# Kernel optimization log

Measured on AMD Instinct MI355X. Metric: run time of the kernel, lower is better.

## Reference

```python
import jax, jax.numpy as jnp
import numpy as np

N, E = 50000, 800000
IN_DIM = 128
OUT_DIM = 128
H = 8
D = OUT_DIM // H  # head_dim = 16
LN_EPS = 1e-5


def setup_inputs() -> dict:
    key = jax.random.key(0)
    ks = jax.random.split(key, 16)
    s_in = 1.0 / np.sqrt(IN_DIM)
    s_out = 1.0 / np.sqrt(OUT_DIM)
    return {
        "x": jax.random.normal(ks[0], (N, IN_DIM), dtype=jnp.float32),
        "edge_index": jax.random.randint(ks[1], (2, E), 0, N, dtype=jnp.int32),
        "edge_attr": jax.random.uniform(ks[2], (E,), dtype=jnp.float32),
        # per-head TransformerConv params, stacked over heads (heads=1 per conv)
        "Wq": jax.random.normal(ks[3], (H, IN_DIM, D), dtype=jnp.float32) * s_in,
        "bq": jnp.zeros((H, D), dtype=jnp.float32),
        "Wk": jax.random.normal(ks[4], (H, IN_DIM, D), dtype=jnp.float32) * s_in,
        "bk": jnp.zeros((H, D), dtype=jnp.float32),
        "Wv": jax.random.normal(ks[5], (H, IN_DIM, D), dtype=jnp.float32) * s_in,
        "bv": jnp.zeros((H, D), dtype=jnp.float32),
        "We": jax.random.normal(ks[6], (H, D), dtype=jnp.float32),  # lin_edge (edge_dim=1, no bias)
        "Wskip": jax.random.normal(ks[7], (H, IN_DIM, D), dtype=jnp.float32) * s_in,
        "bskip": jnp.zeros((H, D), dtype=jnp.float32),
        "Wo": jax.random.normal(ks[8], (OUT_DIM, OUT_DIM), dtype=jnp.float32) * s_out,
        "bo": jnp.zeros((OUT_DIM,), dtype=jnp.float32),
        "gamma": jnp.ones((OUT_DIM,), dtype=jnp.float32),
        "beta": jnp.zeros((OUT_DIM,), dtype=jnp.float32),
    }


def reference(x, edge_index, edge_attr, Wq, bq, Wk, bk, Wv, bv, We, Wskip, bskip, Wo, bo, gamma, beta):
    n = x.shape[0]
    h, _, d = Wq.shape
    src, dst = edge_index[0], edge_index[1]
    # node-level projections for all heads at once: [N, H, D]
    q = jnp.einsum('ni,hid->nhd', x, Wq) + bq
    k = jnp.einsum('ni,hid->nhd', x, Wk) + bk
    v = jnp.einsum('ni,hid->nhd', x, Wv) + bv
    # edge embedding: lin_edge on scalar edge_attr -> [E, H, D]
    e = edge_attr[:, None, None] * We[None, :, :]
    # attention logits per edge/head: q_dst . (k_src + e) / sqrt(d)
    ke = k[src] + e
    alpha = jnp.einsum('ehd,ehd->eh', q[dst], ke) / jnp.sqrt(jnp.asarray(d, x.dtype))
    # segment softmax over destination nodes
    m = jax.ops.segment_max(alpha, dst, num_segments=n)  # [N, H]
    m = jnp.where(jnp.isfinite(m), m, 0.0)
    ex = jnp.exp(alpha - m[dst])
    denom = jax.ops.segment_sum(ex, dst, num_segments=n)
    w = ex / jnp.maximum(denom[dst], 1e-16)  # [E, H]
    # weighted aggregation of (v_src + e)
    agg = jax.ops.segment_sum(w[:, :, None] * (v[src] + e), dst, num_segments=n)  # [N, H, D]
    # root/skip connection inside each TransformerConv
    skip = jnp.einsum('ni,hid->nhd', x, Wskip) + bskip
    heads_cat = (agg + skip).reshape(n, h * d)  # concat over heads -> [N, OUT_DIM]
    out = heads_cat @ Wo + bo
    out = out + x  # residual (in_dim == out_dim)
    mu = out.mean(-1, keepdims=True)
    var = out.var(-1, keepdims=True)
    out = (out - mu) * jax.lax.rsqrt(var + LN_EPS) * gamma + beta
    return out
```

## Files before the change

kernel.cpp:

```cpp
#include <hip/hip_runtime.h>
#include <hip/hip_bf16.h>
#include <stdint.h>
#include <math.h>

#define IN_DIM 128
#define H_HEADS 8
#define HD 16

typedef __attribute__((ext_vector_type(8))) short bf16x8;
typedef __attribute__((ext_vector_type(4))) float f32x4;

__device__ __forceinline__ unsigned short f2bf(float f) {
    __hip_bfloat16 h = __float2bfloat16(f);
    return reinterpret_cast<unsigned short&>(h);
}
__device__ __forceinline__ float bf2f(unsigned short h) {
    return __uint_as_float(((unsigned int)h) << 16);
}

__device__ __forceinline__ void split_f8(const float4 f0, const float4 f1,
                                         bf16x8& h8, bf16x8& l8) {
    float ff[8] = {f0.x, f0.y, f0.z, f0.w, f1.x, f1.y, f1.z, f1.w};
    union { bf16x8 v; unsigned short u[8]; } H, L;
#pragma unroll
    for (int j = 0; j < 8; ++j) {
        H.u[j] = f2bf(ff[j]);
        L.u[j] = f2bf(ff[j] - bf2f(H.u[j]));
    }
    h8 = H.v; l8 = L.v;
}

__device__ __forceinline__ void stage_B(const unsigned short* __restrict__ src,
                                        unsigned short* __restrict__ lds, int t)
{
#pragma unroll
    for (int j = 0; j < 8; ++j) {
        int idx16 = t + j * 256;
        int c = idx16 >> 4, kcol = idx16 & 15;
        uint4 v = *reinterpret_cast<const uint4*>(src + (size_t)c * 128 + kcol * 8);
        *reinterpret_cast<uint4*>(lds + c * 128 + ((kcol ^ (c & 15)) * 8)) = v;
    }
}
__device__ __forceinline__ bf16x8 read_B(const unsigned short* __restrict__ lds,
                                         int c, int kcol)
{
    return *reinterpret_cast<const bf16x8*>(lds + c * 128 + ((kcol ^ (c & 15)) * 8));
}

__global__ __launch_bounds__(256)
void prep_count_kernel(const float* __restrict__ Wq, const float* __restrict__ Wk,
                       const float* __restrict__ Wv, const float* __restrict__ Wsk,
                       const float* __restrict__ Wo,
                       const float* __restrict__ bq, const float* __restrict__ bk,
                       const float* __restrict__ bv, const float* __restrict__ bsk,
                       unsigned short* __restrict__ WtH, unsigned short* __restrict__ WtL,
                       float* __restrict__ bias_cat,
                       const int* __restrict__ ei, int* __restrict__ deg, int E)
{
    const int b = blockIdx.x;
    const int t = threadIdx.x;
    if (b >= 5) {
        int e = (b - 5) * 256 + t;
        if (e < E) atomicAdd(&deg[ei[E + e]], 1);
        return;
    }
    const int p = b;
    const float* src = (p == 0) ? Wq : (p == 1) ? Wk : (p == 2) ? Wv : (p == 3) ? Wsk : Wo;
    unsigned short* dh = WtH + (size_t)p * 16384;
    unsigned short* dl = WtL + (size_t)p * 16384;
#pragma unroll
    for (int j = 0; j < 64; ++j) {
        int o = t + j * 256;
        int c = o >> 7, k = o & 127;
        float v;
        if (p < 4) {
            int h = c >> 4, d = c & 15;
            v = src[(size_t)h * 2048 + (size_t)k * 16 + d];
        } else {
            v = src[(size_t)k * 128 + c];
        }
        unsigned short hi = f2bf(v);
        unsigned short lo = f2bf(v - bf2f(hi));
        dh[o] = hi; dl[o] = lo;
    }
    if (p < 4 && t < 128) {
        const float* bb = (p == 0) ? bq : (p == 1) ? bk : (p == 2) ? bv : bsk;
        bias_cat[p * 128 + t] = bb[t];
    }
}

__global__ __launch_bounds__(256)
void gemm_proj_kernel(const float* __restrict__ A,
                      const unsigned short* __restrict__ WtH_base,
                      const unsigned short* __restrict__ WtL_base,
                      const float* __restrict__ bias_cat,
                      float* __restrict__ qout, float* __restrict__ skipout,
                      unsigned short* __restrict__ kvout, int N)
{
    __shared__ unsigned short Bs[16384];
    const int t = threadIdx.x;
    const int lane = t & 63;
    const int w = t >> 6;
    const int lr = lane & 15;
    const int lk = lane >> 4;
    const int p = blockIdx.y;
    const int brow0 = blockIdx.x * 64 + w * 16;
    const int arow = min(brow0 + lr, N - 1);
    const float* ap = A + (size_t)arow * 128;

    bf16x8 ah[4], al[4];
#pragma unroll
    for (int ks = 0; ks < 4; ++ks) {
        float4 f0 = *reinterpret_cast<const float4*>(ap + ks * 32 + lk * 8);
        float4 f1 = *reinterpret_cast<const float4*>(ap + ks * 32 + lk * 8 + 4);
        split_f8(f0, f1, ah[ks], al[ks]);
    }

    f32x4 acc[8];
#pragma unroll
    for (int ni = 0; ni < 8; ++ni) acc[ni] = (f32x4){0.f, 0.f, 0.f, 0.f};

    stage_B(WtH_base + (size_t)p * 16384, Bs, t);
    __syncthreads();
#pragma unroll
    for (int ks = 0; ks < 4; ++ks)
#pragma unroll
        for (int ni = 0; ni < 8; ++ni) {
            bf16x8 bh = read_B(Bs, ni * 16 + lr, ks * 4 + lk);
            acc[ni] = __builtin_amdgcn_mfma_f32_16x16x32_bf16(ah[ks], bh, acc[ni], 0, 0, 0);
            acc[ni] = __builtin_amdgcn_mfma_f32_16x16x32_bf16(al[ks], bh, acc[ni], 0, 0, 0);
        }
    __syncthreads();
    stage_B(WtL_base + (size_t)p * 16384, Bs, t);
    __syncthreads();
#pragma unroll
    for (int ks = 0; ks < 4; ++ks)
#pragma unroll
        for (int ni = 0; ni < 8; ++ni) {
            bf16x8 bl = read_B(Bs, ni * 16 + lr, ks * 4 + lk);
            acc[ni] = __builtin_amdgcn_mfma_f32_16x16x32_bf16(ah[ks], bl, acc[ni], 0, 0, 0);
        }

    const float* bias = bias_cat + p * 128;
    if (p == 0 || p == 3) {
        float* outp = (p == 0) ? qout : skipout;
#pragma unroll
        for (int ni = 0; ni < 8; ++ni) {
            int col = ni * 16 + lr;
            float bc = bias[col];
#pragma unroll
            for (int r = 0; r < 4; ++r) {
                int gr = brow0 + lk * 4 + r;
                if (gr < N) outp[(size_t)gr * 128 + col] = acc[ni][r] + bc;
            }
        }
    } else {
        unsigned int* kvu = (unsigned int*)kvout;
        const int slot = (p == 1) ? 0 : 1;
#pragma unroll
        for (int ni = 0; ni < 8; ++ni) {
            int col = ni * 16 + lr;
            float bc = bias[col];
#pragma unroll
            for (int r = 0; r < 4; ++r) {
                unsigned int s = f2bf(acc[ni][r] + bc);
                unsigned int o = __shfl_xor((int)s, 1);
                int gr = brow0 + lk * 4 + r;
                if (((lr & 1) == 0) && gr < N)
                    kvu[(size_t)gr * 128 + 2 * (col >> 1) + slot] = s | (o << 16);
            }
        }
    }
}

__global__ __launch_bounds__(256)
void gemm_out_ln_kernel(const float* __restrict__ A,
                        const unsigned short* __restrict__ BtH_t,
                        const unsigned short* __restrict__ BtL_t,
                        const float* __restrict__ bo,
                        const float* __restrict__ res,
                        const float* __restrict__ gamma,
                        const float* __restrict__ beta,
                        float* __restrict__ out, int N)
{
    __shared__ unsigned short Bs[16384];
    __shared__ float lnS[2][32], lnSq[2][32];
    const int t = threadIdx.x;
    const int lane = t & 63;
    const int w = t >> 6;
    const int lr = lane & 15;
    const int lk = lane >> 4;
    const int ch = w & 1;
    const int rg = w >> 1;
    const int brow0 = blockIdx.x * 32 + rg * 16;
    const int arow = min(brow0 + lr, N - 1);
    const float* ap = A + (size_t)arow * 128;

    bf16x8 ah[4], al[4];
#pragma unroll
    for (int ks = 0; ks < 4; ++ks) {
        float4 f0 = *reinterpret_cast<const float4*>(ap + ks * 32 + lk * 8);
        float4 f1 = *reinterpret_cast<const float4*>(ap + ks * 32 + lk * 8 + 4);
        split_f8(f0, f1, ah[ks], al[ks]);
    }

    f32x4 acc[4];
#pragma unroll
    for (int ni = 0; ni < 4; ++ni) acc[ni] = (f32x4){0.f, 0.f, 0.f, 0.f};

    stage_B(BtH_t, Bs, t);
    __syncthreads();
#pragma unroll
    for (int ks = 0; ks < 4; ++ks)
#pragma unroll
        for (int ni = 0; ni < 4; ++ni) {
            bf16x8 bh = read_B(Bs, ch * 64 + ni * 16 + lr, ks * 4 + lk);
            acc[ni] = __builtin_amdgcn_mfma_f32_16x16x32_bf16(ah[ks], bh, acc[ni], 0, 0, 0);
            acc[ni] = __builtin_amdgcn_mfma_f32_16x16x32_bf16(al[ks], bh, acc[ni], 0, 0, 0);
        }
    __syncthreads();
    stage_B(BtL_t, Bs, t);
    __syncthreads();
#pragma unroll
    for (int ks = 0; ks < 4; ++ks)
#pragma unroll
        for (int ni = 0; ni < 4; ++ni) {
            bf16x8 bl = read_B(Bs, ch * 64 + ni * 16 + lr, ks * 4 + lk);
            acc[ni] = __builtin_amdgcn_mfma_f32_16x16x32_bf16(ah[ks], bl, acc[ni], 0, 0, 0);
        }

#pragma unroll
    for (int ni = 0; ni < 4; ++ni) {
        int col = ch * 64 + ni * 16 + lr;
        float bc = bo[col];
#pragma unroll
        for (int r = 0; r < 4; ++r) {
            int gr = brow0 + lk * 4 + r;
            float rv = (gr < N) ? res[(size_t)gr * 128 + col] : 0.f;
            acc[ni][r] += bc + rv;
        }
    }
    float ps[4], pq[4];
#pragma unroll
    for (int r = 0; r < 4; ++r) {
        float s = 0.f, sq = 0.f;
#pragma unroll
        for (int ni = 0; ni < 4; ++ni) { float v = acc[ni][r]; s += v; sq += v * v; }
#pragma unroll
        for (int mk = 1; mk < 16; mk <<= 1) {
            s  += __shfl_xor(s, mk);
            sq += __shfl_xor(sq, mk);
        }
        ps[r] = s; pq[r] = sq;
    }
    if (lr == 0) {
#pragma unroll
        for (int r = 0; r < 4; ++r) {
            lnS [ch][rg * 16 + lk * 4 + r] = ps[r];
            lnSq[ch][rg * 16 + lk * 4 + r] = pq[r];
        }
    }
    __syncthreads();
#pragma unroll
    for (int r = 0; r < 4; ++r) {
        int rib = rg * 16 + lk * 4 + r;
        float s  = lnS [0][rib] + lnS [1][rib];
        float sq = lnSq[0][rib] + lnSq[1][rib];
        float mean = s * (1.0f / 128.0f);
        float var  = sq * (1.0f / 128.0f) - mean * mean;
        float inv  = rsqrtf(var + 1e-5f);
        int gr = brow0 + lk * 4 + r;
        if (gr < N) {
#pragma unroll
            for (int ni = 0; ni < 4; ++ni) {
                int col = ch * 64 + ni * 16 + lr;
                out[(size_t)gr * 128 + col] =
                    (acc[ni][r] - mean) * inv * gamma[col] + beta[col];
            }
        }
    }
}

__global__ __launch_bounds__(1024)
void scan_kernel(const int* __restrict__ deg, int* __restrict__ offs,
                 int* __restrict__ cursor, int N)
{
    __shared__ int wsum[16];
    __shared__ int chunk_total_s;
    const int t = threadIdx.x;
    const int lane = t & 63, wid = t >> 6;
    int running = 0;
    for (int base = 0; base < N; base += 4096) {
        int v[4];
        int idx = base + t * 4;
#pragma unroll
        for (int j = 0; j < 4; ++j) { int i = idx + j; v[j] = (i < N) ? deg[i] : 0; }
        int ls = v[0] + v[1] + v[2] + v[3];
        int inc = ls;
#pragma unroll
        for (int off = 1; off < 64; off <<= 1) {
            int y = __shfl_up(inc, off);
            if (lane >= off) inc += y;
        }
        if (lane == 63) wsum[wid] = inc;
        __syncthreads();
        if (t < 16) {
            int winc = wsum[t];
            for (int off = 1; off < 16; off <<= 1) {
                int y = __shfl_up(winc, off);
                if (t >= off) winc += y;
            }
            wsum[t] = winc;
            if (t == 15) chunk_total_s = winc;
        }
        __syncthreads();
        int wexcl = (wid == 0) ? 0 : wsum[wid - 1];
        int texcl = running + wexcl + (inc - ls);
        int pre = 0;
#pragma unroll
        for (int j = 0; j < 4; ++j) {
            int i = idx + j;
            if (i < N) { offs[i] = texcl + pre; cursor[i] = texcl + pre; }
            pre += v[j];
        }
        running += chunk_total_s;
        __syncthreads();
    }
    if (t == 0) offs[N] = running;
}

__global__ void scatter_kernel(const int* __restrict__ ei, const float* __restrict__ ea,
                               int* __restrict__ cursor, int2* __restrict__ csr, int E)
{
    int e = blockIdx.x * 256 + threadIdx.x;
    if (e < E) {
        int s = ei[e], d = ei[E + e];
        int pos = atomicAdd(&cursor[d], 1);
        csr[pos] = make_int2(s, __float_as_int(ea[e]));
    }
}

__global__ __launch_bounds__(256)
void agg_kernel(const float* __restrict__ qb, const float* __restrict__ sb,
                const unsigned short* __restrict__ kvb,
                const int* __restrict__ offs, const int2* __restrict__ csr,
                const float* __restrict__ We, float* __restrict__ heads_cat, int N)
{
    const int lane = threadIdx.x & 63;
    const int node = blockIdx.x * 4 + (threadIdx.x >> 6);
    if (node >= N) return;
    const int h32 = lane & 31;
    const int half = lane >> 5;

    const float4 q4  = *reinterpret_cast<const float4*>(qb + (size_t)node * 128 + 4 * h32);
    const float4 we4 = *reinterpret_cast<const float4*>(We + 4 * h32);

    float qwe = q4.x * we4.x + q4.y * we4.y + q4.z * we4.z + q4.w * we4.w;
    qwe += __shfl_xor(qwe, 1);
    qwe += __shfl_xor(qwe, 2);

    const int e0 = offs[node];
    const int cnt = offs[node + 1] - e0;
    const int myCnt = (cnt > half) ? ((cnt - half + 1) >> 1) : 0;
    const int2* cp = csr + e0 + half;

    float m = -__builtin_huge_valf();
    float s = 0.f, a0 = 0.f, a1 = 0.f, a2 = 0.f, a3 = 0.f;

#define KVG(ec) (*reinterpret_cast<const uint4*>(kvb + (size_t)(ec).x * 256 + 8 * h32))
#define PROC(ec, u) do { \
    float eav_ = __int_as_float((ec).y); \
    float k0_ = __uint_as_float((u).x << 16); \
    float k1_ = __uint_as_float((u).x & 0xffff0000u); \
    float k2_ = __uint_as_float((u).z << 16); \
    float k3_ = __uint_as_float((u).z & 0xffff0000u); \
    float part_ = q4.x * k0_ + q4.y * k1_ + q4.z * k2_ + q4.w * k3_; \
    part_ += __shfl_xor(part_, 1); \
    part_ += __shfl_xor(part_, 2); \
    float alpha_ = (part_ + eav_ * qwe) * 0.25f; \
    float d_ = alpha_ - m; \
    float e_ = __expf(-fabsf(d_)); \
    bool up_ = d_ > 0.f; \
    float pv_ = up_ ? 1.f : e_; \
    float sc_ = up_ ? e_ : 1.f; \
    m = up_ ? alpha_ : m; \
    float t_ = pv_ * eav_; \
    float v0_ = __uint_as_float((u).y << 16); \
    float v1_ = __uint_as_float((u).y & 0xffff0000u); \
    float v2_ = __uint_as_float((u).w << 16); \
    float v3_ = __uint_as_float((u).w & 0xffff0000u); \
    s  = fmaf(s,  sc_, pv_); \
    a0 = fmaf(a0, sc_, fmaf(t_, we4.x, pv_ * v0_)); \
    a1 = fmaf(a1, sc_, fmaf(t_, we4.y, pv_ * v1_)); \
    a2 = fmaf(a2, sc_, fmaf(t_, we4.z, pv_ * v2_)); \
    a3 = fmaf(a3, sc_, fmaf(t_, we4.w, pv_ * v3_)); \
} while (0)

    int2 c0v, c1v, cnv;
    uint4 g0v, g1v;
    if (myCnt > 0) c0v = cp[0];
    if (myCnt > 1) c1v = cp[2];
    if (myCnt > 0) g0v = KVG(c0v);
    if (myCnt > 1) g1v = KVG(c1v);

    for (int j = 0; j < myCnt; ++j) {
        if (j + 2 < myCnt) cnv = cp[2 * j + 4];
        PROC(c0v, g0v);
        c0v = c1v; g0v = g1v; c1v = cnv;
        if (j + 2 < myCnt) g1v = KVG(c1v);
    }

    float om = __shfl_xor(m, 32);
    float os = __shfl_xor(s, 32);
    float o0 = __shfl_xor(a0, 32);
    float o1 = __shfl_xor(a1, 32);
    float o2 = __shfl_xor(a2, 32);
    float o3 = __shfl_xor(a3, 32);
    float nm = fmaxf(m, om);
    float eS = (s  > 0.f) ? __expf(m  - nm) : 0.f;
    float eO = (os > 0.f) ? __expf(om - nm) : 0.f;
    float st = s * eS + os * eO;
    float r0 = a0 * eS + o0 * eO;
    float r1 = a1 * eS + o1 * eO;
    float r2 = a2 * eS + o2 * eO;
    float r3 = a3 * eS + o3 * eO;

    if (half == 0) {
        float inv = 1.0f / fmaxf(st, 1e-16f);
        const float4 sk = *reinterpret_cast<const float4*>(sb + (size_t)node * 128 + 4 * h32);
        float4 o;
        o.x = r0 * inv + sk.x;
        o.y = r1 * inv + sk.y;
        o.z = r2 * inv + sk.z;
        o.w = r3 * inv + sk.w;
        *reinterpret_cast<float4*>(heads_cat + (size_t)node * 128 + 4 * h32) = o;
    }
#undef KVG
#undef PROC
}

extern "C" void kernel_launch(void* const* d_in, const int* in_sizes, int n_in,
                              void* d_out, int out_size, void* d_ws, size_t ws_size,
                              hipStream_t stream)
{
    const float* x    = (const float*)d_in[0];
    const int*   ei   = (const int*)d_in[1];
    const float* ea   = (const float*)d_in[2];
    const float* Wq   = (const float*)d_in[3];
    const float* bq   = (const float*)d_in[4];
    const float* Wk   = (const float*)d_in[5];
    const float* bk   = (const float*)d_in[6];
    const float* Wv   = (const float*)d_in[7];
    const float* bv   = (const float*)d_in[8];
    const float* We   = (const float*)d_in[9];
    const float* Wsk  = (const float*)d_in[10];
    const float* bsk  = (const float*)d_in[11];
    const float* Wo   = (const float*)d_in[12];
    const float* bo   = (const float*)d_in[13];
    const float* gamma= (const float*)d_in[14];
    const float* beta = (const float*)d_in[15];
    const int N = in_sizes[0] / 128;
    const int E = in_sizes[1] / 2;
    float* out = (float*)d_out;

    char* w = (char*)d_ws;
    float* qarr      = (float*)w; w += (size_t)N * 128 * sizeof(float);
    float* skiparr   = (float*)w; w += (size_t)N * 128 * sizeof(float);
    unsigned short* kv = (unsigned short*)w; w += (size_t)N * 256 * sizeof(unsigned short);
    float* heads_cat = (float*)w; w += (size_t)N * 128 * sizeof(float);
    int*   deg       = (int*)w;   w += ((size_t)N + 16) * sizeof(int);
    int*   offs      = (int*)w;   w += ((size_t)N + 16) * sizeof(int);
    int*   cursor    = (int*)w;   w += ((size_t)N + 16) * sizeof(int);
    int2*  csr       = (int2*)w;  w += (size_t)E * sizeof(int2);
    unsigned short* WtH = (unsigned short*)w; w += (size_t)5 * 16384 * sizeof(unsigned short);
    unsigned short* WtL = (unsigned short*)w; w += (size_t)5 * 16384 * sizeof(unsigned short);
    float* bias_cat  = (float*)w; w += 4 * 128 * sizeof(float);

    hipMemsetAsync(deg, 0, (size_t)N * sizeof(int), stream);

    const int cntBlocks = (E + 255) / 256;
    prep_count_kernel<<<5 + cntBlocks, 256, 0, stream>>>(Wq, Wk, Wv, Wsk, Wo, bq, bk, bv, bsk,
                                                         WtH, WtL, bias_cat, ei, deg, E);

    dim3 gProj((N + 63) / 64, 4);
    gemm_proj_kernel<<<gProj, 256, 0, stream>>>(x, WtH, WtL, bias_cat, qarr, skiparr, kv, N);

    scan_kernel<<<1, 1024, 0, stream>>>(deg, offs, cursor, N);
    scatter_kernel<<<(E + 255) / 256, 256, 0, stream>>>(ei, ea, cursor, csr, E);
    agg_kernel<<<(N + 3) / 4, 256, 0, stream>>>(qarr, skiparr, kv, offs, csr, We, heads_cat, N);

    gemm_out_ln_kernel<<<(N + 31) / 32, 256, 0, stream>>>(heads_cat,
                                                          WtH + (size_t)4 * 16384,
                                                          WtL + (size_t)4 * 16384,
                                                          bo, x, gamma, beta, out, N);
}
```

Before: 357.0 us.

## Parallelize CSR scan, lazy-rescale softmax in aggregation, widen output GEMM rows per wave

The single-block serial scan becomes a three-kernel multi-block scan. The aggregation kernel now factors the edge-embedding term out of the per-edge accumulation into one weighted sum of edge attributes. It also only rescales the running softmax state when a logit exceeds the max by more than 8, and prefetches deeper. The output GEMM+LayerNorm kernel now gives each wave a full 128-column row tile, so the LDS cross-wave reduction and one barrier go away, at the cost of more accumulator registers. The lazy max threshold risks precision if exponents grow large, and the extra scan launches add launch overhead.

```diff
diff --git a/kernel.cpp b/kernel.cpp
--- a/kernel.cpp
+++ b/kernel.cpp
@@ -184,15 +184,12 @@
                         float* __restrict__ out, int N)
 {
     __shared__ unsigned short Bs[16384];
-    __shared__ float lnS[2][32], lnSq[2][32];
     const int t = threadIdx.x;
     const int lane = t & 63;
     const int w = t >> 6;
     const int lr = lane & 15;
     const int lk = lane >> 4;
-    const int ch = w & 1;
-    const int rg = w >> 1;
-    const int brow0 = blockIdx.x * 32 + rg * 16;
+    const int brow0 = blockIdx.x * 64 + w * 16;
     const int arow = min(brow0 + lr, N - 1);
     const float* ap = A + (size_t)arow * 128;
 
@@ -204,17 +201,17 @@
         split_f8(f0, f1, ah[ks], al[ks]);
     }
 
-    f32x4 acc[4];
-#pragma unroll
-    for (int ni = 0; ni < 4; ++ni) acc[ni] = (f32x4){0.f, 0.f, 0.f, 0.f};
+    f32x4 acc[8];
+#pragma unroll
+    for (int ni = 0; ni < 8; ++ni) acc[ni] = (f32x4){0.f, 0.f, 0.f, 0.f};
 
     stage_B(BtH_t, Bs, t);
     __syncthreads();
 #pragma unroll
     for (int ks = 0; ks < 4; ++ks)
 #pragma unroll
-        for (int ni = 0; ni < 4; ++ni) {
-            bf16x8 bh = read_B(Bs, ch * 64 + ni * 16 + lr, ks * 4 + lk);
+        for (int ni = 0; ni < 8; ++ni) {
+            bf16x8 bh = read_B(Bs, ni * 16 + lr, ks * 4 + lk);
             acc[ni] = __builtin_amdgcn_mfma_f32_16x16x32_bf16(ah[ks], bh, acc[ni], 0, 0, 0);
             acc[ni] = __builtin_amdgcn_mfma_f32_16x16x32_bf16(al[ks], bh, acc[ni], 0, 0, 0);
         }
@@ -224,14 +221,14 @@
 #pragma unroll
     for (int ks = 0; ks < 4; ++ks)
 #pragma unroll
-        for (int ni = 0; ni < 4; ++ni) {
-            bf16x8 bl = read_B(Bs, ch * 64 + ni * 16 + lr, ks * 4 + lk);
+        for (int ni = 0; ni < 8; ++ni) {
+            bf16x8 bl = read_B(Bs, ni * 16 + lr, ks * 4 + lk);
             acc[ni] = __builtin_amdgcn_mfma_f32_16x16x32_bf16(ah[ks], bl, acc[ni], 0, 0, 0);
         }
 
 #pragma unroll
-    for (int ni = 0; ni < 4; ++ni) {
-        int col = ch * 64 + ni * 16 + lr;
+    for (int ni = 0; ni < 8; ++ni) {
+        int col = ni * 16 + lr;
         float bc = bo[col];
 #pragma unroll
         for (int r = 0; r < 4; ++r) {
@@ -240,40 +237,24 @@
             acc[ni][r] += bc + rv;
         }
     }
-    float ps[4], pq[4];
 #pragma unroll
     for (int r = 0; r < 4; ++r) {
         float s = 0.f, sq = 0.f;
 #pragma unroll
-        for (int ni = 0; ni < 4; ++ni) { float v = acc[ni][r]; s += v; sq += v * v; }
+        for (int ni = 0; ni < 8; ++ni) { float v = acc[ni][r]; s += v; sq += v * v; }
 #pragma unroll
         for (int mk = 1; mk < 16; mk <<= 1) {
             s  += __shfl_xor(s, mk);
             sq += __shfl_xor(sq, mk);
         }
-        ps[r] = s; pq[r] = sq;
-    }
-    if (lr == 0) {
-#pragma unroll
-        for (int r = 0; r < 4; ++r) {
-            lnS [ch][rg * 16 + lk * 4 + r] = ps[r];
-            lnSq[ch][rg * 16 + lk * 4 + r] = pq[r];
-        }
-    }
-    __syncthreads();
-#pragma unroll
-    for (int r = 0; r < 4; ++r) {
-        int rib = rg * 16 + lk * 4 + r;
-        float s  = lnS [0][rib] + lnS [1][rib];
-        float sq = lnSq[0][rib] + lnSq[1][rib];
         float mean = s * (1.0f / 128.0f);
         float var  = sq * (1.0f / 128.0f) - mean * mean;
         float inv  = rsqrtf(var + 1e-5f);
         int gr = brow0 + lk * 4 + r;
         if (gr < N) {
 #pragma unroll
-            for (int ni = 0; ni < 4; ++ni) {
-                int col = ch * 64 + ni * 16 + lr;
+            for (int ni = 0; ni < 8; ++ni) {
+                int col = ni * 16 + lr;
                 out[(size_t)gr * 128 + col] =
                     (acc[ni][r] - mean) * inv * gamma[col] + beta[col];
             }
@@ -282,51 +263,73 @@
 }
 
 __global__ __launch_bounds__(1024)
-void scan_kernel(const int* __restrict__ deg, int* __restrict__ offs,
-                 int* __restrict__ cursor, int N)
+void scan_part1(const int* __restrict__ deg, int* __restrict__ offs,
+                int* __restrict__ csums, int N)
 {
     __shared__ int wsum[16];
-    __shared__ int chunk_total_s;
     const int t = threadIdx.x;
     const int lane = t & 63, wid = t >> 6;
-    int running = 0;
-    for (int base = 0; base < N; base += 4096) {
-        int v[4];
-        int idx = base + t * 4;
-#pragma unroll
-        for (int j = 0; j < 4; ++j) { int i = idx + j; v[j] = (i < N) ? deg[i] : 0; }
-        int ls = v[0] + v[1] + v[2] + v[3];
-        int inc = ls;
-#pragma unroll
-        for (int off = 1; off < 64; off <<= 1) {
-            int y = __shfl_up(inc, off);
-            if (lane >= off) inc += y;
-        }
-        if (lane == 63) wsum[wid] = inc;
-        __syncthreads();
-        if (t < 16) {
-            int winc = wsum[t];
-            for (int off = 1; off < 16; off <<= 1) {
-                int y = __shfl_up(winc, off);
-                if (t >= off) winc += y;
-            }
-            wsum[t] = winc;
-            if (t == 15) chunk_total_s = winc;
-        }
-        __syncthreads();
-        int wexcl = (wid == 0) ? 0 : wsum[wid - 1];
-        int texcl = running + wexcl + (inc - ls);
-        int pre = 0;
-#pragma unroll
-        for (int j = 0; j < 4; ++j) {
-            int i = idx + j;
-            if (i < N) { offs[i] = texcl + pre; cursor[i] = texcl + pre; }
-            pre += v[j];
-        }
-        running += chunk_total_s;
-        __syncthreads();
-    }
-    if (t == 0) offs[N] = running;
+    const int idx = blockIdx.x * 4096 + t * 4;
+    int v[4];
+#pragma unroll
+    for (int j = 0; j < 4; ++j) { int i = idx + j; v[j] = (i < N) ? deg[i] : 0; }
+    int ls = v[0] + v[1] + v[2] + v[3];
+    int inc = ls;
+#pragma unroll
+    for (int off = 1; off < 64; off <<= 1) {
+        int y = __shfl_up(inc, off);
+        if (lane >= off) inc += y;
+    }
+    if (lane == 63) wsum[wid] = inc;
+    __syncthreads();
+    if (t < 16) {
+        int winc = wsum[t];
+        for (int off = 1; off < 16; off <<= 1) {
+            int y = __shfl_up(winc, off);
+            if (t >= off) winc += y;
+        }
+        wsum[t] = winc;
+    }
+    __syncthreads();
+    int wexcl = (wid == 0) ? 0 : wsum[wid - 1];
+    int texcl = wexcl + (inc - ls);
+    int pre = 0;
+#pragma unroll
+    for (int j = 0; j < 4; ++j) {
+        int i = idx + j;
+        if (i < N) offs[i] = texcl + pre;
+        pre += v[j];
+    }
+    if (t == 0) csums[blockIdx.x] = wsum[15];
+}
+
+__global__ void scan_part2(int* __restrict__ csums, int nc,
+                           int* __restrict__ offs, int N)
+{
+    const int t = threadIdx.x;
+    int v = (t < nc) ? csums[t] : 0;
+    int inc = v;
+#pragma unroll
+    for (int off = 1; off < 64; off <<= 1) {
+        int y = __shfl_up(inc, off);
+        if (t >= off) inc += y;
+    }
+    if (t < nc) csums[t] = inc - v;
+    int total = __shfl(inc, nc - 1);
+    if (t == 0) offs[N] = total;
+}
+
+__global__ __launch_bounds__(1024)
+void scan_part3(int* __restrict__ offs, const int* __restrict__ csums,
+                int* __restrict__ cursor, int N)
+{
+    const int coff = csums[blockIdx.x];
+    const int idx = blockIdx.x * 4096 + threadIdx.x * 4;
+#pragma unroll
+    for (int j = 0; j < 4; ++j) {
+        int i = idx + j;
+        if (i < N) { int val = offs[i] + coff; offs[i] = val; cursor[i] = val; }
+    }
 }
 
 __global__ void scatter_kernel(const int* __restrict__ ei, const float* __restrict__ ea,
@@ -365,61 +368,66 @@
     const int2* cp = csr + e0 + half;
 
     float m = -__builtin_huge_valf();
-    float s = 0.f, a0 = 0.f, a1 = 0.f, a2 = 0.f, a3 = 0.f;
+    float s = 0.f, sWE = 0.f, a0 = 0.f, a1 = 0.f, a2 = 0.f, a3 = 0.f;
 
 #define KVG(ec) (*reinterpret_cast<const uint4*>(kvb + (size_t)(ec).x * 256 + 8 * h32))
-#define PROC(ec, u) do { \
-    float eav_ = __int_as_float((ec).y); \
-    float k0_ = __uint_as_float((u).x << 16); \
-    float k1_ = __uint_as_float((u).x & 0xffff0000u); \
-    float k2_ = __uint_as_float((u).z << 16); \
-    float k3_ = __uint_as_float((u).z & 0xffff0000u); \
-    float part_ = q4.x * k0_ + q4.y * k1_ + q4.z * k2_ + q4.w * k3_; \
-    part_ += __shfl_xor(part_, 1); \
-    part_ += __shfl_xor(part_, 2); \
-    float alpha_ = (part_ + eav_ * qwe) * 0.25f; \
-    float d_ = alpha_ - m; \
-    float e_ = __expf(-fabsf(d_)); \
-    bool up_ = d_ > 0.f; \
-    float pv_ = up_ ? 1.f : e_; \
-    float sc_ = up_ ? e_ : 1.f; \
-    m = up_ ? alpha_ : m; \
-    float t_ = pv_ * eav_; \
-    float v0_ = __uint_as_float((u).y << 16); \
-    float v1_ = __uint_as_float((u).y & 0xffff0000u); \
-    float v2_ = __uint_as_float((u).w << 16); \
-    float v3_ = __uint_as_float((u).w & 0xffff0000u); \
-    s  = fmaf(s,  sc_, pv_); \
-    a0 = fmaf(a0, sc_, fmaf(t_, we4.x, pv_ * v0_)); \
-    a1 = fmaf(a1, sc_, fmaf(t_, we4.y, pv_ * v1_)); \
-    a2 = fmaf(a2, sc_, fmaf(t_, we4.z, pv_ * v2_)); \
-    a3 = fmaf(a3, sc_, fmaf(t_, we4.w, pv_ * v3_)); \
-} while (0)
-
-    int2 c0v, c1v, cnv;
-    uint4 g0v, g1v;
-    if (myCnt > 0) c0v = cp[0];
-    if (myCnt > 1) c1v = cp[2];
-    if (myCnt > 0) g0v = KVG(c0v);
-    if (myCnt > 1) g1v = KVG(c1v);
+
+    int2 c0, c1, c2, c3;
+    uint4 g0, g1, g2;
+    if (myCnt > 0) c0 = cp[0];
+    if (myCnt > 1) c1 = cp[2];
+    if (myCnt > 2) c2 = cp[4];
+    if (myCnt > 3) c3 = cp[6];
+    if (myCnt > 0) g0 = KVG(c0);
+    if (myCnt > 1) g1 = KVG(c1);
+    if (myCnt > 2) g2 = KVG(c2);
 
     for (int j = 0; j < myCnt; ++j) {
-        if (j + 2 < myCnt) cnv = cp[2 * j + 4];
-        PROC(c0v, g0v);
-        c0v = c1v; g0v = g1v; c1v = cnv;
-        if (j + 2 < myCnt) g1v = KVG(c1v);
-    }
-
-    float om = __shfl_xor(m, 32);
-    float os = __shfl_xor(s, 32);
-    float o0 = __shfl_xor(a0, 32);
-    float o1 = __shfl_xor(a1, 32);
-    float o2 = __shfl_xor(a2, 32);
-    float o3 = __shfl_xor(a3, 32);
+        const float eav = __int_as_float(c0.y);
+        float k0 = __uint_as_float(g0.x << 16);
+        float k1 = __uint_as_float(g0.x & 0xffff0000u);
+        float k2 = __uint_as_float(g0.z << 16);
+        float k3 = __uint_as_float(g0.z & 0xffff0000u);
+        float part = q4.x * k0 + q4.y * k1 + q4.z * k2 + q4.w * k3;
+        part += __shfl_xor(part, 1);
+        part += __shfl_xor(part, 2);
+        float alpha = fmaf(eav, qwe, part) * 0.25f;
+        float d = alpha - m;
+        if (__any(d > 8.f)) {
+            float nm = fmaxf(m, alpha);
+            float sc = __expf(m - nm);
+            m = nm; d = alpha - m;
+            s *= sc; sWE *= sc; a0 *= sc; a1 *= sc; a2 *= sc; a3 *= sc;
+        }
+        float pv = __expf(d);
+        s += pv;
+        sWE = fmaf(pv, eav, sWE);
+        float v0 = __uint_as_float(g0.y << 16);
+        float v1 = __uint_as_float(g0.y & 0xffff0000u);
+        float v2 = __uint_as_float(g0.w << 16);
+        float v3 = __uint_as_float(g0.w & 0xffff0000u);
+        a0 = fmaf(pv, v0, a0);
+        a1 = fmaf(pv, v1, a1);
+        a2 = fmaf(pv, v2, a2);
+        a3 = fmaf(pv, v3, a3);
+        c0 = c1; c1 = c2; c2 = c3;
+        g0 = g1; g1 = g2;
+        if (j + 4 < myCnt) c3 = cp[2 * j + 8];
+        if (j + 3 < myCnt) g2 = KVG(c2);
+    }
+
+    float om  = __shfl_xor(m, 32);
+    float os  = __shfl_xor(s, 32);
+    float oWE = __shfl_xor(sWE, 32);
+    float o0  = __shfl_xor(a0, 32);
+    float o1  = __shfl_xor(a1, 32);
+    float o2  = __shfl_xor(a2, 32);
+    float o3  = __shfl_xor(a3, 32);
     float nm = fmaxf(m, om);
     float eS = (s  > 0.f) ? __expf(m  - nm) : 0.f;
     float eO = (os > 0.f) ? __expf(om - nm) : 0.f;
-    float st = s * eS + os * eO;
+    float st  = s * eS + os * eO;
+    float SWE = sWE * eS + oWE * eO;
     float r0 = a0 * eS + o0 * eO;
     float r1 = a1 * eS + o1 * eO;
     float r2 = a2 * eS + o2 * eO;
@@ -429,14 +437,13 @@
         float inv = 1.0f / fmaxf(st, 1e-16f);
         const float4 sk = *reinterpret_cast<const float4*>(sb + (size_t)node * 128 + 4 * h32);
         float4 o;
-        o.x = r0 * inv + sk.x;
-        o.y = r1 * inv + sk.y;
-        o.z = r2 * inv + sk.z;
-        o.w = r3 * inv + sk.w;
+        o.x = fmaf(SWE, we4.x, r0) * inv + sk.x;
+        o.y = fmaf(SWE, we4.y, r1) * inv + sk.y;
+        o.z = fmaf(SWE, we4.z, r2) * inv + sk.z;
+        o.w = fmaf(SWE, we4.w, r3) * inv + sk.w;
         *reinterpret_cast<float4*>(heads_cat + (size_t)node * 128 + 4 * h32) = o;
     }
 #undef KVG
-#undef PROC
 }
 
 extern "C" void kernel_launch(void* const* d_in, const int* in_sizes, int n_in,
@@ -471,6 +478,7 @@
     int*   deg       = (int*)w;   w += ((size_t)N + 16) * sizeof(int);
     int*   offs      = (int*)w;   w += ((size_t)N + 16) * sizeof(int);
     int*   cursor    = (int*)w;   w += ((size_t)N + 16) * sizeof(int);
+    int*   csums     = (int*)w;   w += 256 * sizeof(int);
     int2*  csr       = (int2*)w;  w += (size_t)E * sizeof(int2);
     unsigned short* WtH = (unsigned short*)w; w += (size_t)5 * 16384 * sizeof(unsigned short);
     unsigned short* WtL = (unsigned short*)w; w += (size_t)5 * 16384 * sizeof(unsigned short);
@@ -485,11 +493,15 @@
     dim3 gProj((N + 63) / 64, 4);
     gemm_proj_kernel<<<gProj, 256, 0, stream>>>(x, WtH, WtL, bias_cat, qarr, skiparr, kv, N);
 
-    scan_kernel<<<1, 1024, 0, stream>>>(deg, offs, cursor, N);
+    const int nChunks = (N + 4095) / 4096;
+    scan_part1<<<nChunks, 1024, 0, stream>>>(deg, offs, csums, N);
+    scan_part2<<<1, 64, 0, stream>>>(csums, nChunks, offs, N);
+    scan_part3<<<nChunks, 1024, 0, stream>>>(offs, csums, cursor, N);
+
     scatter_kernel<<<(E + 255) / 256, 256, 0, stream>>>(ei, ea, cursor, csr, E);
     agg_kernel<<<(N + 3) / 4, 256, 0, stream>>>(qarr, skiparr, kv, offs, csr, We, heads_cat, N);
 
-    gemm_out_ln_kernel<<<(N + 31) / 32, 256, 0, stream>>>(heads_cat,
+    gemm_out_ln_kernel<<<(N + 63) / 64, 256, 0, stream>>>(heads_cat,
                                                           WtH + (size_t)4 * 16384,
                                                           WtL + (size_t)4 * 16384,
                                                           bo, x, gamma, beta, out, N);
```

Result: faster. 326.3 us (-8.6%).
